# Kernel tuning notes

Hardware: AMD Instinct MI355X
Metric: run time of the kernel (lower is better)

## Reference

```python
import jax, jax.numpy as jnp
import numpy as np

N_IN, N_OUT, H = 32, 31, 128
B1, B2 = 256, 256


def setup_inputs() -> dict:
    key = jax.random.key(0)
    ks = jax.random.split(key, 6)
    def lin(k, o, i):
        return jax.random.normal(k, (o, i), jnp.float32) / np.float32(np.sqrt(i))
    return {
        "t": jax.random.uniform(ks[0], (), jnp.float32),
        "y": jax.random.normal(ks[1], (B1, B2, N_OUT), jnp.float32),
        "W0": lin(ks[2], H, N_IN), "b0": jnp.zeros((H,), jnp.float32),
        "W1": lin(ks[3], H, H),    "b1": jnp.zeros((H,), jnp.float32),
        "W2": lin(ks[4], H, H),    "b2": jnp.zeros((H,), jnp.float32),
        "W3": lin(ks[5], N_OUT, H), "b3": jnp.zeros((N_OUT,), jnp.float32),
    }


def reference(t, y, W0, b0, W1, b1, W2, b2, W3, b3):
    # inp[..., :-1] = y ; inp[..., -1] = force(t) with force = sin
    force = jnp.sin(t)
    inp = jnp.concatenate(
        [y, jnp.broadcast_to(force, y.shape[:-1] + (1,))], axis=-1
    )  # [B1, B2, N_IN]

    def model(x):  # x: [N_IN]
        h = jnp.tanh(W0 @ x + b0)
        h = jnp.tanh(W1 @ h + b1)
        h = jnp.tanh(W2 @ h + b2)
        return W3 @ h + b3  # [N_OUT]

    out = jax.vmap(jax.vmap(model))(inp)  # [B1, B2, N_OUT]
    # vmap(vmap(jacrev(model)))(inp)[..., :-1] -> drop d/d(force) column
    jac = jax.vmap(jax.vmap(jax.jacrev(model)))(inp)[..., :-1]  # [B1,B2,N_OUT,N_IN-1]
    return out, jac
```

## Files before the change

### kernel.cpp

```cpp
#include <hip/hip_runtime.h>
#include <hip/hip_bf16.h>
#include <math.h>


using short8 = __attribute__((ext_vector_type(8))) short;
using f32x4  = __attribute__((ext_vector_type(4))) float;

#define PB 4
#define PPB 32
#define STRIDE 136
#define ST3 136

__device__ __forceinline__ float fast_tanh(float z) {
    float e = __expf(2.0f * z);
    return 1.0f - 2.0f * __builtin_amdgcn_rcpf(e + 1.0f);
}

__device__ __forceinline__ unsigned pk2(float lo, float hi) {
    unsigned r;
    asm("v_cvt_pk_bf16_f32 %0, %1, %2" : "=v"(r) : "v"(lo), "v"(hi));
    return r;
}

__device__ __forceinline__ float bf2f(ushort u) {
    union { unsigned u; float f; } c; c.u = ((unsigned)u) << 16; return c.f;
}

__device__ __forceinline__ ushort f2bf1(float f) {
    union { float f; unsigned u; } v; v.f = f;
    unsigned r = v.u + 0x7fffu + ((v.u >> 16) & 1u);
    return (ushort)(r >> 16);
}

__device__ __forceinline__ short8 pack8f(const float* s) {
    union { unsigned u[4]; short8 v; } r;
    #pragma unroll
    for (int qq = 0; qq < 4; ++qq) r.u[qq] = pk2(s[2 * qq], s[2 * qq + 1]);
    return r.v;
}

__device__ __forceinline__ short8 load_row8(const float* p) {
    float tmp[8];
    const float4* p4 = reinterpret_cast<const float4*>(p);
    float4 q0 = p4[0], q1 = p4[1];
    tmp[0]=q0.x; tmp[1]=q0.y; tmp[2]=q0.z; tmp[3]=q0.w;
    tmp[4]=q1.x; tmp[5]=q1.y; tmp[6]=q1.z; tmp[7]=q1.w;
    return pack8f(tmp);
}

__global__ void __launch_bounds__(512, 2)
node_mfma(const float* __restrict__ tptr,
          const float* __restrict__ y,
          const float* __restrict__ W0, const float* __restrict__ b0,
          const float* __restrict__ W1, const float* __restrict__ b1,
          const float* __restrict__ W2, const float* __restrict__ b2,
          const float* __restrict__ W3, const float* __restrict__ b3,
          float* __restrict__ out, float* __restrict__ jac, int npts) {
    __shared__ __align__(16) ushort XT[2][PB][32][STRIDE];
    __shared__ __align__(16) ushort W3L[32 * ST3];
    __shared__ __align__(16) ushort bb12[2][128];
    __shared__ __align__(16) ushort b3L[32];
    __shared__ float xb[PB][32];

    const int tid  = threadIdx.x;
    const int w    = tid >> 6;
    const int lane = tid & 63;
    const int r16  = lane & 15;
    const int g    = lane >> 4;
    const int j    = 16 * w + r16;
    const int q    = w & 3;
    const int pg   = w >> 2;

    {
        int row = tid >> 4, ch = tid & 15;
        float tmp[8];
        if (row < 31) {
            const float4* p4 = reinterpret_cast<const float4*>(W3 + row * 128 + ch * 8);
            float4 q0 = p4[0], q1 = p4[1];
            tmp[0]=q0.x; tmp[1]=q0.y; tmp[2]=q0.z; tmp[3]=q0.w;
            tmp[4]=q1.x; tmp[5]=q1.y; tmp[6]=q1.z; tmp[7]=q1.w;
        } else {
            #pragma unroll
            for (int i = 0; i < 8; ++i) tmp[i] = 0.0f;
        }
        *reinterpret_cast<short8*>(&W3L[row * ST3 + ch * 8]) = pack8f(tmp);
    }
    if (tid < 256) {
        int L = tid >> 7, i = tid & 127;
        bb12[L][i] = f2bf1((L ? b2 : b1)[i]);
    }
    if (tid < 32) b3L[tid] = (tid < 31) ? f2bf1(b3[tid]) : (ushort)0;

    float w0f[8];
    {
        const float4* p4 = reinterpret_cast<const float4*>(W0 + j * 32 + g * 8);
        float4 q0 = p4[0], q1 = p4[1];
        w0f[0]=q0.x; w0f[1]=q0.y; w0f[2]=q0.z; w0f[3]=q0.w;
        w0f[4]=q1.x; w0f[5]=q1.y; w0f[6]=q1.z; w0f[7]=q1.w;
    }
    short8 aW[2][2][4];
    #pragma unroll
    for (int mt = 0; mt < 2; ++mt) {
        const int row = 16 * q + 64 * mt + r16;
        #pragma unroll
        for (int kc = 0; kc < 4; ++kc) {
            aW[0][mt][kc] = load_row8(W1 + row * 128 + kc * 32 + g * 8);
            aW[1][mt][kc] = load_row8(W2 + row * 128 + kc * 32 + g * 8);
        }
    }
    const int mw = (w >> 1) & 1, nw = w & 1;
    const float b0v = b0[j];
    const float force = sinf(tptr[0]);

    const int pl0 = tid >> 5, c0 = tid & 31;
    const bool act = tid < PB * 32;
    float pf = 0.0f;
    if (act && c0 < 31) pf = y[(size_t)(blockIdx.x * PPB + pl0) * 31 + c0];

    for (int pass = 0; pass < PPB / PB; ++pass) {
        const int pbase = blockIdx.x * PPB + pass * PB;

        if (act) xb[pl0][c0] = (c0 < 31) ? pf : force;
        __syncthreads();

        #pragma unroll
        for (int pl = 0; pl < PB; ++pl) {
            float zp = 0.0f;
            #pragma unroll
            for (int i = 0; i < 8; ++i) zp = fmaf(w0f[i], xb[pl][g * 8 + i], zp);
            zp += __shfl_xor(zp, 16, 64);
            zp += __shfl_xor(zp, 32, 64);
            float h = fast_tanh(zp + b0v);
            float d = 1.0f - h * h;
            #pragma unroll
            for (int i = 0; i < 8; ++i) {
                int c = g * 8 + i;
                XT[0][pl][c][j] = f2bf1((c == 31) ? h : d * w0f[i]);
            }
        }

        if (act && c0 < 31 && pass + 1 < PPB / PB)
            pf = y[(size_t)(pbase + PB + pl0) * 31 + c0];

        __syncthreads();

        #pragma unroll
        for (int L = 0; L < 2; ++L) {
            #pragma unroll
            for (int pi = 0; pi < 2; ++pi) {
                const int pl = 2 * pg + pi;
                f32x4 acc[2][2] = {{{0.f,0.f,0.f,0.f},{0.f,0.f,0.f,0.f}},
                                   {{0.f,0.f,0.f,0.f},{0.f,0.f,0.f,0.f}}};
                __builtin_amdgcn_s_setprio(1);
                #pragma unroll
                for (int kc = 0; kc < 4; ++kc) {
                    short8 bf0 = *reinterpret_cast<const short8*>(&XT[L][pl][r16][kc * 32 + g * 8]);
                    short8 bf1 = *reinterpret_cast<const short8*>(&XT[L][pl][16 + r16][kc * 32 + g * 8]);
                    acc[0][0] = __builtin_amdgcn_mfma_f32_16x16x32_bf16(aW[L][0][kc], bf0, acc[0][0], 0, 0, 0);
                    acc[0][1] = __builtin_amdgcn_mfma_f32_16x16x32_bf16(aW[L][0][kc], bf1, acc[0][1], 0, 0, 0);
                    acc[1][0] = __builtin_amdgcn_mfma_f32_16x16x32_bf16(aW[L][1][kc], bf0, acc[1][0], 0, 0, 0);
                    acc[1][1] = __builtin_amdgcn_mfma_f32_16x16x32_bf16(aW[L][1][kc], bf1, acc[1][1], 0, 0, 0);
                }
                __builtin_amdgcn_s_setprio(0);
                #pragma unroll
                for (int mt = 0; mt < 2; ++mt) {
                    uint2 bq = *reinterpret_cast<const uint2*>(&bb12[L][16 * q + 64 * mt + 4 * g]);
                    const ushort* bqs = reinterpret_cast<const ushort*>(&bq);
                    float va[4], vb[4];
                    #pragma unroll
                    for (int reg = 0; reg < 4; ++reg) {
                        float tv = fast_tanh(acc[mt][1][reg] + bf2f(bqs[reg]));
                        float d  = 1.0f - tv * tv;
                        float dd = __shfl(d, lane | 15, 64);
                        va[reg] = dd * acc[mt][0][reg];
                        vb[reg] = (r16 == 15) ? tv : dd * acc[mt][1][reg];
                    }
                    uint2 pa, pb;
                    pa.x = pk2(va[0], va[1]); pa.y = pk2(va[2], va[3]);
                    pb.x = pk2(vb[0], vb[1]); pb.y = pk2(vb[2], vb[3]);
                    const int col = 16 * q + 64 * mt + 4 * g;
                    *reinterpret_cast<uint2*>(&XT[1 - L][pl][r16][col])      = pa;
                    *reinterpret_cast<uint2*>(&XT[1 - L][pl][16 + r16][col]) = pb;
                }
            }
            __syncthreads();
        }

        uint2 b3q = *reinterpret_cast<const uint2*>(&b3L[16 * mw + 4 * g]);
        const ushort* b3s = reinterpret_cast<const ushort*>(&b3q);
        #pragma unroll
        for (int tsk = 0; tsk < 2; ++tsk) {
            int pl = (w >> 2) + tsk * 2;
            f32x4 a = {0.f, 0.f, 0.f, 0.f};
            __builtin_amdgcn_s_setprio(1);
            #pragma unroll
            for (int kc = 0; kc < 4; ++kc) {
                short8 aw3 = *reinterpret_cast<const short8*>(&W3L[(16 * mw + r16) * ST3 + kc * 32 + g * 8]);
                short8 bf  = *reinterpret_cast<const short8*>(&XT[0][pl][16 * nw + r16][kc * 32 + g * 8]);
                a = __builtin_amdgcn_mfma_f32_16x16x32_bf16(aw3, bf, a, 0, 0, 0);
            }
            __builtin_amdgcn_s_setprio(0);
            size_t p = (size_t)(pbase + pl);
            int c = 16 * nw + r16;
            if ((int)p < npts) {
                #pragma unroll
                for (int reg = 0; reg < 4; ++reg) {
                    int o = 16 * mw + 4 * g + reg;
                    if (o < 31) {
                        if (c == 31) out[p * 31 + o] = a[reg] + bf2f(b3s[reg]);
                        else         jac[(p * 31 + o) * 31 + c] = a[reg];
                    }
                }
            }
        }
    }
}

extern "C" void kernel_launch(void* const* d_in, const int* in_sizes, int n_in,
                              void* d_out, int out_size, void* d_ws, size_t ws_size,
                              hipStream_t stream) {
    const float* t  = (const float*)d_in[0];
    const float* y  = (const float*)d_in[1];
    const float* W0 = (const float*)d_in[2];
    const float* b0 = (const float*)d_in[3];
    const float* W1 = (const float*)d_in[4];
    const float* b1 = (const float*)d_in[5];
    const float* W2 = (const float*)d_in[6];
    const float* b2 = (const float*)d_in[7];
    const float* W3 = (const float*)d_in[8];
    const float* b3 = (const float*)d_in[9];

    const int npts = in_sizes[1] / 31;
    float* out = (float*)d_out;
    float* jac = out + (size_t)npts * 31;

    const int blocks = (npts + PPB - 1) / PPB;
    node_mfma<<<blocks, 512, 0, stream>>>(t, y, W0, b0, W1, b1, W2, b2, W3, b3,
                                          out, jac, npts);
}
```

Before: 402.0 us.

## Compute first layer with MFMA via one-hot identity tiles and shrink points per block

Replaces the scalar per-lane first-layer dot product and its shuffle reduction with MFMA calls. W0 is multiplied by a B operand built from one-hot identity columns plus the input vector, so the layer's activation and its tangent columns come out of the same MFMA tile and reuse the shared epilogue. Points per pass drop from 4 to 2 and points per block from 32 to 16, giving more blocks and one point per wave group. The tradeoff is bf16 rounding of the input and layer-0 bias, and more blocks each reloading the weights.

```diff
diff --git a/kernel.cpp b/kernel.cpp
--- a/kernel.cpp
+++ b/kernel.cpp
@@ -6,39 +6,35 @@
 using short8 = __attribute__((ext_vector_type(8))) short;
 using f32x4  = __attribute__((ext_vector_type(4))) float;
 
-#define PB 4
-#define PPB 32
-#define STRIDE 136
+#define PB 2
+#define PPB 16
+#define NPASS (PPB / PB)
+#define ST 136
 #define ST3 136
 
 __device__ __forceinline__ float fast_tanh(float z) {
     float e = __expf(2.0f * z);
     return 1.0f - 2.0f * __builtin_amdgcn_rcpf(e + 1.0f);
 }
-
 __device__ __forceinline__ unsigned pk2(float lo, float hi) {
     unsigned r;
     asm("v_cvt_pk_bf16_f32 %0, %1, %2" : "=v"(r) : "v"(lo), "v"(hi));
     return r;
 }
-
 __device__ __forceinline__ float bf2f(ushort u) {
     union { unsigned u; float f; } c; c.u = ((unsigned)u) << 16; return c.f;
 }
-
 __device__ __forceinline__ ushort f2bf1(float f) {
     union { float f; unsigned u; } v; v.f = f;
     unsigned r = v.u + 0x7fffu + ((v.u >> 16) & 1u);
     return (ushort)(r >> 16);
 }
-
 __device__ __forceinline__ short8 pack8f(const float* s) {
     union { unsigned u[4]; short8 v; } r;
     #pragma unroll
     for (int qq = 0; qq < 4; ++qq) r.u[qq] = pk2(s[2 * qq], s[2 * qq + 1]);
     return r.v;
 }
-
 __device__ __forceinline__ short8 load_row8(const float* p) {
     float tmp[8];
     const float4* p4 = reinterpret_cast<const float4*>(p);
@@ -56,20 +52,20 @@
           const float* __restrict__ W2, const float* __restrict__ b2,
           const float* __restrict__ W3, const float* __restrict__ b3,
           float* __restrict__ out, float* __restrict__ jac, int npts) {
-    __shared__ __align__(16) ushort XT[2][PB][32][STRIDE];
+    __shared__ __align__(16) ushort XT[2][PB][32][ST];
     __shared__ __align__(16) ushort W3L[32 * ST3];
-    __shared__ __align__(16) ushort bb12[2][128];
+    __shared__ __align__(16) ushort bbf[3][128];
     __shared__ __align__(16) ushort b3L[32];
-    __shared__ float xb[PB][32];
+    __shared__ __align__(16) float xb[PB][32];
 
     const int tid  = threadIdx.x;
     const int w    = tid >> 6;
     const int lane = tid & 63;
     const int r16  = lane & 15;
     const int g    = lane >> 4;
-    const int j    = 16 * w + r16;
     const int q    = w & 3;
-    const int pg   = w >> 2;
+    const int pt   = w >> 2;
+    const int mw   = (w >> 1) & 1, nw = w & 1;
 
     {
         int row = tid >> 4, ch = tid & 15;
@@ -85,127 +81,134 @@
         }
         *reinterpret_cast<short8*>(&W3L[row * ST3 + ch * 8]) = pack8f(tmp);
     }
-    if (tid < 256) {
+    if (tid < 384) {
         int L = tid >> 7, i = tid & 127;
-        bb12[L][i] = f2bf1((L ? b2 : b1)[i]);
+        bbf[L][i] = f2bf1((L == 0 ? b0 : L == 1 ? b1 : b2)[i]);
     }
     if (tid < 32) b3L[tid] = (tid < 31) ? f2bf1(b3[tid]) : (ushort)0;
 
-    float w0f[8];
-    {
-        const float4* p4 = reinterpret_cast<const float4*>(W0 + j * 32 + g * 8);
-        float4 q0 = p4[0], q1 = p4[1];
-        w0f[0]=q0.x; w0f[1]=q0.y; w0f[2]=q0.z; w0f[3]=q0.w;
-        w0f[4]=q1.x; w0f[5]=q1.y; w0f[6]=q1.z; w0f[7]=q1.w;
-    }
+    short8 aW0[2];
     short8 aW[2][2][4];
     #pragma unroll
     for (int mt = 0; mt < 2; ++mt) {
         const int row = 16 * q + 64 * mt + r16;
+        aW0[mt] = load_row8(W0 + row * 32 + g * 8);
         #pragma unroll
         for (int kc = 0; kc < 4; ++kc) {
             aW[0][mt][kc] = load_row8(W1 + row * 128 + kc * 32 + g * 8);
             aW[1][mt][kc] = load_row8(W2 + row * 128 + kc * 32 + g * 8);
         }
     }
-    const int mw = (w >> 1) & 1, nw = w & 1;
-    const float b0v = b0[j];
+
+    short8 oh0, oh1;
+    {
+        union { ushort u[8]; short8 v; } z0, z1;
+        #pragma unroll
+        for (int i = 0; i < 8; ++i) {
+            z0.u[i] = (g == (r16 >> 3) && i == (r16 & 7)) ? (ushort)0x3F80 : (ushort)0;
+            z1.u[i] = (r16 < 15 && g == ((16 + r16) >> 3) && i == ((16 + r16) & 7))
+                          ? (ushort)0x3F80 : (ushort)0;
+        }
+        oh0 = z0.v; oh1 = z1.v;
+    }
+
     const float force = sinf(tptr[0]);
 
+    const bool act = tid < PB * 32;
     const int pl0 = tid >> 5, c0 = tid & 31;
-    const bool act = tid < PB * 32;
     float pf = 0.0f;
     if (act && c0 < 31) pf = y[(size_t)(blockIdx.x * PPB + pl0) * 31 + c0];
 
-    for (int pass = 0; pass < PPB / PB; ++pass) {
+    auto epi = [&](f32x4 a0, f32x4 a1, int mt, const ushort* bL, ushort* dst) {
+        const int row0 = 16 * q + 64 * mt;
+        uint2 bq = *reinterpret_cast<const uint2*>(&bL[row0 + 4 * g]);
+        const ushort* bqs = reinterpret_cast<const ushort*>(&bq);
+        float va[4], vb[4];
+        #pragma unroll
+        for (int reg = 0; reg < 4; ++reg) {
+            float tv = fast_tanh(a1[reg] + bf2f(bqs[reg]));
+            float d  = 1.0f - tv * tv;
+            float dd = __shfl(d, lane | 15, 64);
+            va[reg] = dd * a0[reg];
+            vb[reg] = (r16 == 15) ? tv : dd * a1[reg];
+        }
+        uint2 pa, pb;
+        pa.x = pk2(va[0], va[1]); pa.y = pk2(va[2], va[3]);
+        pb.x = pk2(vb[0], vb[1]); pb.y = pk2(vb[2], vb[3]);
+        *reinterpret_cast<uint2*>(&dst[r16 * ST + row0 + 4 * g])        = pa;
+        *reinterpret_cast<uint2*>(&dst[(16 + r16) * ST + row0 + 4 * g]) = pb;
+    };
+
+    for (int pass = 0; pass < NPASS; ++pass) {
         const int pbase = blockIdx.x * PPB + pass * PB;
 
         if (act) xb[pl0][c0] = (c0 < 31) ? pf : force;
         __syncthreads();
 
-        #pragma unroll
-        for (int pl = 0; pl < PB; ++pl) {
-            float zp = 0.0f;
+        {
+            float xa[8];
+            const float4* xp = reinterpret_cast<const float4*>(&xb[pt][g * 8]);
+            float4 x0 = xp[0], x1 = xp[1];
+            xa[0]=x0.x; xa[1]=x0.y; xa[2]=x0.z; xa[3]=x0.w;
+            xa[4]=x1.x; xa[5]=x1.y; xa[6]=x1.z; xa[7]=x1.w;
+            short8 xpk = pack8f(xa);
+            short8 bf0 = oh0;
+            short8 bf1 = (r16 == 15) ? xpk : oh1;
+            f32x4 a00 = {0.f,0.f,0.f,0.f}, a01 = {0.f,0.f,0.f,0.f};
+            f32x4 a10 = {0.f,0.f,0.f,0.f}, a11 = {0.f,0.f,0.f,0.f};
+            __builtin_amdgcn_s_setprio(1);
+            a00 = __builtin_amdgcn_mfma_f32_16x16x32_bf16(aW0[0], bf0, a00, 0, 0, 0);
+            a01 = __builtin_amdgcn_mfma_f32_16x16x32_bf16(aW0[0], bf1, a01, 0, 0, 0);
+            a10 = __builtin_amdgcn_mfma_f32_16x16x32_bf16(aW0[1], bf0, a10, 0, 0, 0);
+            a11 = __builtin_amdgcn_mfma_f32_16x16x32_bf16(aW0[1], bf1, a11, 0, 0, 0);
+            __builtin_amdgcn_s_setprio(0);
+            epi(a00, a01, 0, bbf[0], &XT[0][pt][0][0]);
+            epi(a10, a11, 1, bbf[0], &XT[0][pt][0][0]);
+        }
+
+        if (act && c0 < 31 && pass + 1 < NPASS)
+            pf = y[(size_t)(pbase + PB + pl0) * 31 + c0];
+
+        __syncthreads();
+
+        #pragma unroll
+        for (int L = 0; L < 2; ++L) {
+            f32x4 acc[2][2] = {{{0.f,0.f,0.f,0.f},{0.f,0.f,0.f,0.f}},
+                               {{0.f,0.f,0.f,0.f},{0.f,0.f,0.f,0.f}}};
+            __builtin_amdgcn_s_setprio(1);
             #pragma unroll
-            for (int i = 0; i < 8; ++i) zp = fmaf(w0f[i], xb[pl][g * 8 + i], zp);
-            zp += __shfl_xor(zp, 16, 64);
-            zp += __shfl_xor(zp, 32, 64);
-            float h = fast_tanh(zp + b0v);
-            float d = 1.0f - h * h;
-            #pragma unroll
-            for (int i = 0; i < 8; ++i) {
-                int c = g * 8 + i;
-                XT[0][pl][c][j] = f2bf1((c == 31) ? h : d * w0f[i]);
+            for (int kc = 0; kc < 4; ++kc) {
+                short8 bf0 = *reinterpret_cast<const short8*>(&XT[L][pt][r16][kc * 32 + g * 8]);
+                short8 bf1 = *reinterpret_cast<const short8*>(&XT[L][pt][16 + r16][kc * 32 + g * 8]);
+                acc[0][0] = __builtin_amdgcn_mfma_f32_16x16x32_bf16(aW[L][0][kc], bf0, acc[0][0], 0, 0, 0);
+                acc[0][1] = __builtin_amdgcn_mfma_f32_16x16x32_bf16(aW[L][0][kc], bf1, acc[0][1], 0, 0, 0);
+                acc[1][0] = __builtin_amdgcn_mfma_f32_16x16x32_bf16(aW[L][1][kc], bf0, acc[1][0], 0, 0, 0);
+                acc[1][1] = __builtin_amdgcn_mfma_f32_16x16x32_bf16(aW[L][1][kc], bf1, acc[1][1], 0, 0, 0);
             }
-        }
-
-        if (act && c0 < 31 && pass + 1 < PPB / PB)
-            pf = y[(size_t)(pbase + PB + pl0) * 31 + c0];
-
-        __syncthreads();
-
-        #pragma unroll
-        for (int L = 0; L < 2; ++L) {
-            #pragma unroll
-            for (int pi = 0; pi < 2; ++pi) {
-                const int pl = 2 * pg + pi;
-                f32x4 acc[2][2] = {{{0.f,0.f,0.f,0.f},{0.f,0.f,0.f,0.f}},
-                                   {{0.f,0.f,0.f,0.f},{0.f,0.f,0.f,0.f}}};
-                __builtin_amdgcn_s_setprio(1);
-                #pragma unroll
-                for (int kc = 0; kc < 4; ++kc) {
-                    short8 bf0 = *reinterpret_cast<const short8*>(&XT[L][pl][r16][kc * 32 + g * 8]);
-                    short8 bf1 = *reinterpret_cast<const short8*>(&XT[L][pl][16 + r16][kc * 32 + g * 8]);
-                    acc[0][0] = __builtin_amdgcn_mfma_f32_16x16x32_bf16(aW[L][0][kc], bf0, acc[0][0], 0, 0, 0);
-                    acc[0][1] = __builtin_amdgcn_mfma_f32_16x16x32_bf16(aW[L][0][kc], bf1, acc[0][1], 0, 0, 0);
-                    acc[1][0] = __builtin_amdgcn_mfma_f32_16x16x32_bf16(aW[L][1][kc], bf0, acc[1][0], 0, 0, 0);
-                    acc[1][1] = __builtin_amdgcn_mfma_f32_16x16x32_bf16(aW[L][1][kc], bf1, acc[1][1], 0, 0, 0);
-                }
-                __builtin_amdgcn_s_setprio(0);
-                #pragma unroll
-                for (int mt = 0; mt < 2; ++mt) {
-                    uint2 bq = *reinterpret_cast<const uint2*>(&bb12[L][16 * q + 64 * mt + 4 * g]);
-                    const ushort* bqs = reinterpret_cast<const ushort*>(&bq);
-                    float va[4], vb[4];
-                    #pragma unroll
-                    for (int reg = 0; reg < 4; ++reg) {
-                        float tv = fast_tanh(acc[mt][1][reg] + bf2f(bqs[reg]));
-                        float d  = 1.0f - tv * tv;
-                        float dd = __shfl(d, lane | 15, 64);
-                        va[reg] = dd * acc[mt][0][reg];
-                        vb[reg] = (r16 == 15) ? tv : dd * acc[mt][1][reg];
-                    }
-                    uint2 pa, pb;
-                    pa.x = pk2(va[0], va[1]); pa.y = pk2(va[2], va[3]);
-                    pb.x = pk2(vb[0], vb[1]); pb.y = pk2(vb[2], vb[3]);
-                    const int col = 16 * q + 64 * mt + 4 * g;
-                    *reinterpret_cast<uint2*>(&XT[1 - L][pl][r16][col])      = pa;
-                    *reinterpret_cast<uint2*>(&XT[1 - L][pl][16 + r16][col]) = pb;
-                }
-            }
+            __builtin_amdgcn_s_setprio(0);
+            epi(acc[0][0], acc[0][1], 0, bbf[L + 1], &XT[1 - L][pt][0][0]);
+            epi(acc[1][0], acc[1][1], 1, bbf[L + 1], &XT[1 - L][pt][0][0]);
             __syncthreads();
         }
 
-        uint2 b3q = *reinterpret_cast<const uint2*>(&b3L[16 * mw + 4 * g]);
-        const ushort* b3s = reinterpret_cast<const ushort*>(&b3q);
-        #pragma unroll
-        for (int tsk = 0; tsk < 2; ++tsk) {
-            int pl = (w >> 2) + tsk * 2;
+        {
+            uint2 b3q = *reinterpret_cast<const uint2*>(&b3L[16 * mw + 4 * g]);
+            const ushort* b3s = reinterpret_cast<const ushort*>(&b3q);
             f32x4 a = {0.f, 0.f, 0.f, 0.f};
             __builtin_amdgcn_s_setprio(1);
             #pragma unroll
             for (int kc = 0; kc < 4; ++kc) {
                 short8 aw3 = *reinterpret_cast<const short8*>(&W3L[(16 * mw + r16) * ST3 + kc * 32 + g * 8]);
-                short8 bf  = *reinterpret_cast<const short8*>(&XT[0][pl][16 * nw + r16][kc * 32 + g * 8]);
+                short8 bf  = *reinterpret_cast<const short8*>(&XT[0][pt][16 * nw + r16][kc * 32 + g * 8]);
                 a = __builtin_amdgcn_mfma_f32_16x16x32_bf16(aw3, bf, a, 0, 0, 0);
             }
             __builtin_amdgcn_s_setprio(0);
-            size_t p = (size_t)(pbase + pl);
-            int c = 16 * nw + r16;
+            const size_t p = (size_t)(pbase + pt);
+            const int c = 16 * nw + r16;
             if ((int)p < npts) {
                 #pragma unroll
                 for (int reg = 0; reg < 4; ++reg) {
-                    int o = 16 * mw + 4 * g + reg;
+                    const int o = 16 * mw + 4 * g + reg;
                     if (o < 31) {
                         if (c == 31) out[p * 31 + o] = a[reg] + bf2f(b3s[reg]);
                         else         jac[(p * 31 + o) * 31 + c] = a[reg];
```

Measured after the change: 508.6 us. 26.5% more time.
